# Kernel tuning notes

Hardware: AMD Instinct MI355X
Metric: run time of the kernel (lower is better)

The kernel has to match this reference:

```python
import jax, jax.numpy as jnp
import numpy as np

# Brevitas-style per-tensor affine (symmetric) quantization:
#   scale = max|x| / qmax  (stats-derived, treated as constant)
#   q     = clamp(round(x/scale), qmin, qmax) * scale

def _quant_pt(x, bits):
    qmax = 2.0 ** (bits - 1) - 1.0
    qmin = -(2.0 ** (bits - 1))
    scale = jax.lax.stop_gradient(jnp.max(jnp.abs(x))) / qmax
    scale = jnp.maximum(scale, jnp.asarray(1e-8, x.dtype))
    q = jnp.clip(jnp.round(x / scale), qmin, qmax)
    return q * scale, scale


def setup_inputs() -> dict:
    key = jax.random.key(0)
    k1, k2, k3 = jax.random.split(key, 3)
    in_features, out_features, tokens = 4096, 4096, 8192
    inp = jax.random.normal(k1, (tokens, in_features), dtype=jnp.float32)
    # Kaiming-ish init for linear weight [out, in]
    W = jax.random.normal(k2, (out_features, in_features), dtype=jnp.float32) / np.sqrt(in_features)
    b = jax.random.normal(k3, (out_features,), dtype=jnp.float32) * 0.01
    return {"inp": inp, "W": W, "b": b}


def reference(inp, W, b):
    # input quant: Int8 act per-tensor (QuantIdentity default)
    x_dq, s_in = _quant_pt(inp, 8)
    # weight quant: 4-bit per-tensor
    w_dq, s_w = _quant_pt(W, 4)
    # bias quant: Int32 with scale = s_in * s_w
    s_b = s_in * s_w
    b_dq = jnp.round(b / s_b) * s_b  # int32 range never clips realistic biases
    # matmul in dequantized domain (numerically equal to int GEMM * s_in*s_w)
    y = jnp.einsum('ti,oi->to', x_dq, w_dq) + b_dq
    # output quant: Int8 act per-tensor
    y_dq, _ = _quant_pt(y, 8)
    return y_dq
```

## Files before the change

kernel.cpp:

```cpp
#include <hip/hip_runtime.h>


typedef int v4i __attribute__((ext_vector_type(4)));

#define AS1(p) ((const __attribute__((address_space(1))) void*)(p))
#define AS3(p) ((__attribute__((address_space(3))) void*)(p))

#define GM 8192
#define GN 4096
#define GK 4096
#define NBN 16
#define NWG 512

__global__ __launch_bounds__(256) void maxabs_kernel(const float* __restrict__ x, int n4,
                                                     unsigned* __restrict__ slot) {
  __shared__ float red[4];
  int tid = blockIdx.x * blockDim.x + threadIdx.x;
  int stride = gridDim.x * blockDim.x;
  float m = 0.0f;
  const float4* x4 = (const float4*)x;
  for (int i = tid; i < n4; i += stride) {
    float4 v = x4[i];
    m = fmaxf(m, fmaxf(fmaxf(fabsf(v.x), fabsf(v.y)), fmaxf(fabsf(v.z), fabsf(v.w))));
  }
  for (int off = 32; off; off >>= 1) m = fmaxf(m, __shfl_xor(m, off));
  if ((threadIdx.x & 63) == 0) red[threadIdx.x >> 6] = m;
  __syncthreads();
  if (threadIdx.x == 0) {
    float b = fmaxf(fmaxf(red[0], red[1]), fmaxf(red[2], red[3]));
    atomicMax(slot, __float_as_uint(b));
  }
}

__global__ __launch_bounds__(256) void quant_kernel(const float* __restrict__ x,
                                                    signed char* __restrict__ q, int n4,
                                                    const unsigned* __restrict__ slot,
                                                    float qmaxv, float qlo, float qhi) {
  float s = fmaxf(__uint_as_float(*slot) / qmaxv, 1e-8f);
  float inv = 1.0f / s;
  int tid = blockIdx.x * blockDim.x + threadIdx.x;
  int stride = gridDim.x * blockDim.x;
  const float4* x4 = (const float4*)x;
  int* q4 = (int*)q;
  for (int i = tid; i < n4; i += stride) {
    float4 v = x4[i];
    int a0 = (int)fminf(fmaxf(rintf(v.x * inv), qlo), qhi);
    int a1 = (int)fminf(fmaxf(rintf(v.y * inv), qlo), qhi);
    int a2 = (int)fminf(fmaxf(rintf(v.z * inv), qlo), qhi);
    int a3 = (int)fminf(fmaxf(rintf(v.w * inv), qlo), qhi);
    q4[i] = (a0 & 255) | ((a1 & 255) << 8) | ((a2 & 255) << 16) | ((a3 & 255) << 24);
  }
}

__global__ __launch_bounds__(512, 2) void gemm_i8_kernel(const signed char* __restrict__ Xq,
                                                         const signed char* __restrict__ Wq,
                                                         const float* __restrict__ bias,
                                                         const unsigned* __restrict__ slots,
                                                         float* __restrict__ Y,
                                                         unsigned* __restrict__ maxY) {
  __shared__ signed char smem[131072];
  const int tid = threadIdx.x;
  const int wid = tid >> 6, lane = tid & 63;
  const int wr = wid >> 2, wc = wid & 3;
  const int lr = lane & 15, lg = lane >> 4;

  const int bid = (int)blockIdx.x;
  const int swz = (bid & 7) * (NWG / 8) + (bid >> 3);
  const int brow = (swz / NBN) * 256;
  const int bcol = (swz % NBN) * 256;

  const int srr = tid >> 3;
  const int sgl = (tid & 7) ^ (srr & 7);

#define ASLOT(db, h) (smem + ((db) * 2 + (h)) * 16384)
#define BSLOT(db, h) (smem + 65536 + ((db) * 2 + (h)) * 16384)
#define STAGE(gptr, grow0, kofs, slot)                                                        \
  {                                                                                           \
    const signed char* _s0 = (gptr) + (size_t)((grow0) + srr) * GK + (kofs) + sgl * 16;       \
    __builtin_amdgcn_global_load_lds(AS1(_s0), AS3((slot) + wid * 1024), 16, 0, 0);           \
    __builtin_amdgcn_global_load_lds(AS1(_s0 + (size_t)64 * GK),                              \
                                     AS3((slot) + 8192 + wid * 1024), 16, 0, 0);              \
  }

  STAGE(Xq, brow, 0, ASLOT(0, 0));
  STAGE(Wq, bcol, 0, BSLOT(0, 0));
  STAGE(Xq, brow + 128, 0, ASLOT(0, 1));
  STAGE(Wq, bcol + 128, 0, BSLOT(0, 1));
  STAGE(Xq, brow, 128, ASLOT(1, 0));
  STAGE(Wq, bcol, 128, BSLOT(1, 0));

  v4i acc[8][4] = {};

#pragma unroll 2
  for (int t = 0; t < 32; ++t) {
    const int db = t & 1;
    if (t == 31)
      asm volatile("s_waitcnt vmcnt(0)" ::: "memory");
    else
      asm volatile("s_waitcnt vmcnt(4)" ::: "memory");
    __builtin_amdgcn_s_barrier();
#pragma unroll
    for (int q = 0; q < 4; ++q) {
      const int mh = q >> 1, nh = q & 1;
      const signed char* Abuf = ASLOT(db, mh);
      const signed char* Bbuf = BSLOT(db, nh);
      v4i af[4][2], bf[2][2];
#pragma unroll
      for (int mm = 0; mm < 4; ++mm) {
        int hr = wr * 64 + mm * 16 + lr;
        int sw = hr & 7;
#pragma unroll
        for (int kk = 0; kk < 2; ++kk)
          af[mm][kk] = *(const v4i*)(Abuf + hr * 128 + (((kk * 4 + lg) ^ sw) << 4));
      }
#pragma unroll
      for (int nn = 0; nn < 2; ++nn) {
        int hr = wc * 32 + nn * 16 + lr;
        int sw = hr & 7;
#pragma unroll
        for (int kk = 0; kk < 2; ++kk)
          bf[nn][kk] = *(const v4i*)(Bbuf + hr * 128 + (((kk * 4 + lg) ^ sw) << 4));
      }
      if (q == 0 && t + 1 < 32) STAGE(Xq, brow + 128, (t + 1) * 128, ASLOT((t + 1) & 1, 1));
      if (q == 1 && t + 1 < 32) STAGE(Wq, bcol + 128, (t + 1) * 128, BSLOT((t + 1) & 1, 1));
      if (q == 2 && t + 2 < 32) STAGE(Xq, brow, (t + 2) * 128, ASLOT(db, 0));
      if (q == 3 && t + 2 < 32) STAGE(Wq, bcol, (t + 2) * 128, BSLOT(db, 0));
      __builtin_amdgcn_s_barrier();
      asm volatile("s_waitcnt lgkmcnt(0)");
      __builtin_amdgcn_s_setprio(1);
#pragma unroll
      for (int mm = 0; mm < 4; ++mm)
#pragma unroll
        for (int nn = 0; nn < 2; ++nn)
#pragma unroll
          for (int kk = 0; kk < 2; ++kk)
            acc[mh * 4 + mm][nh * 2 + nn] = __builtin_amdgcn_mfma_i32_16x16x64_i8(
                af[mm][kk], bf[nn][kk], acc[mh * 4 + mm][nh * 2 + nn], 0, 0, 0);
      __builtin_amdgcn_s_setprio(0);
      __builtin_amdgcn_s_barrier();
    }
  }

  float s_in = fmaxf(__uint_as_float(slots[0]) / 127.0f, 1e-8f);
  float s_w = fmaxf(__uint_as_float(slots[1]) / 7.0f, 1e-8f);
  float s_b = s_in * s_w;
  float lmax = 0.0f;
#pragma unroll
  for (int n = 0; n < 4; ++n) {
    int o = bcol + (n >> 1) * 128 + wc * 32 + (n & 1) * 16 + lr;
    float bdq = rintf(bias[o] / s_b) * s_b;
#pragma unroll
    for (int m = 0; m < 8; ++m) {
      int t0 = brow + (m >> 2) * 128 + wr * 64 + (m & 3) * 16 + (lg << 2);
#pragma unroll
      for (int r2 = 0; r2 < 4; ++r2) {
        float yv = (float)acc[m][n][r2] * s_b + bdq;
        Y[(size_t)(t0 + r2) * GN + o] = yv;
        lmax = fmaxf(lmax, fabsf(yv));
      }
    }
  }
  for (int off = 32; off; off >>= 1) lmax = fmaxf(lmax, __shfl_xor(lmax, off));
  float* fred = (float*)smem;
  if (lane == 0) fred[wid] = lmax;
  __syncthreads();
  if (tid == 0) {
    float m = fred[0];
#pragma unroll
    for (int i = 1; i < 8; ++i) m = fmaxf(m, fred[i]);
    atomicMax(maxY, __float_as_uint(m));
  }
#undef STAGE
#undef ASLOT
#undef BSLOT
}

__global__ __launch_bounds__(256) void quant_out_kernel(float* __restrict__ y, int n4,
                                                        const unsigned* __restrict__ slot) {
  float s = fmaxf(__uint_as_float(*slot) / 127.0f, 1e-8f);
  float inv = 1.0f / s;
  int tid = blockIdx.x * blockDim.x + threadIdx.x;
  int stride = gridDim.x * blockDim.x;
  float4* y4 = (float4*)y;
  for (int i = tid; i < n4; i += stride) {
    float4 v = y4[i];
    v.x = fminf(fmaxf(rintf(v.x * inv), -128.0f), 127.0f) * s;
    v.y = fminf(fmaxf(rintf(v.y * inv), -128.0f), 127.0f) * s;
    v.z = fminf(fmaxf(rintf(v.z * inv), -128.0f), 127.0f) * s;
    v.w = fminf(fmaxf(rintf(v.w * inv), -128.0f), 127.0f) * s;
    y4[i] = v;
  }
}

extern "C" void kernel_launch(void* const* d_in, const int* in_sizes, int n_in,
                              void* d_out, int out_size, void* d_ws, size_t ws_size,
                              hipStream_t stream) {
  const float* inp = (const float*)d_in[0];
  const float* W = (const float*)d_in[1];
  const float* b = (const float*)d_in[2];
  float* out = (float*)d_out;

  unsigned* slots = (unsigned*)d_ws;
  signed char* Xq = (signed char*)d_ws + 256;
  signed char* Wq = Xq + (size_t)GM * GK;

  const int nX = GM * GK;
  const int nW = GN * GK;

  hipMemsetAsync(d_ws, 0, 16, stream);

  maxabs_kernel<<<1024, 256, 0, stream>>>(inp, nX / 4, slots + 0);
  maxabs_kernel<<<512, 256, 0, stream>>>(W, nW / 4, slots + 1);

  quant_kernel<<<1024, 256, 0, stream>>>(inp, Xq, nX / 4, slots + 0, 127.0f, -128.0f, 127.0f);
  quant_kernel<<<512, 256, 0, stream>>>(W, Wq, nW / 4, slots + 1, 7.0f, -8.0f, 7.0f);

  gemm_i8_kernel<<<NWG, 512, 0, stream>>>(Xq, Wq, b, slots, out, slots + 2);

  quant_out_kernel<<<1024, 256, 0, stream>>>(out, (GM * GN) / 4, slots + 2);
}
```

Before: 286.0 us.

## Restructure int8 GEMM main loop into k-split phases with reused B fragments

Reorders the GEMM inner loop into four phases split by K-half, not by M/N quadrant. B fragments for all four N sub-tiles are loaded once per K-half and reused across both M halves, which cuts LDS reads. Prefetch changes from a two-deep lookahead to a one-ahead double buffer, with stage issues spread across the phases and a vmcnt(2) wait. Shared-memory address offsets are precomputed. The shallower prefetch may expose more global-load latency.

```diff
diff --git a/kernel.cpp b/kernel.cpp
--- a/kernel.cpp
+++ b/kernel.cpp
@@ -72,6 +72,20 @@
   const int srr = tid >> 3;
   const int sgl = (tid & 7) ^ (srr & 7);
 
+  int aoff[4], asw[4], boff[4], bsw[4];
+#pragma unroll
+  for (int mm = 0; mm < 4; ++mm) {
+    int hr = wr * 64 + mm * 16 + lr;
+    aoff[mm] = hr * 128;
+    asw[mm] = hr & 7;
+  }
+#pragma unroll
+  for (int nn = 0; nn < 4; ++nn) {
+    int hr = wc * 32 + (nn & 1) * 16 + lr;
+    boff[nn] = hr * 128;
+    bsw[nn] = hr & 7;
+  }
+
 #define ASLOT(db, h) (smem + ((db) * 2 + (h)) * 16384)
 #define BSLOT(db, h) (smem + 65536 + ((db) * 2 + (h)) * 16384)
 #define STAGE(gptr, grow0, kofs, slot)                                                        \
@@ -81,64 +95,68 @@
     __builtin_amdgcn_global_load_lds(AS1(_s0 + (size_t)64 * GK),                              \
                                      AS3((slot) + 8192 + wid * 1024), 16, 0, 0);              \
   }
-
+#define LDA(mm, db, h, kk) \
+  *(const v4i*)(ASLOT(db, h) + aoff[mm] + ((((kk)*4 + lg) ^ asw[mm]) << 4))
+#define LDB(nn, db, kk) \
+  *(const v4i*)(BSLOT(db, (nn) >> 1) + boff[nn] + ((((kk)*4 + lg) ^ bsw[nn]) << 4))
+#define MFMA16(arow)                                                                          \
+  __builtin_amdgcn_s_setprio(1);                                                              \
+  _Pragma("unroll") for (int mm = 0; mm < 4; ++mm)                                            \
+      _Pragma("unroll") for (int nn = 0; nn < 4; ++nn)                                        \
+          acc[(arow) + mm][nn] =                                                              \
+      __builtin_amdgcn_mfma_i32_16x16x64_i8(af[mm], bf[nn], acc[(arow) + mm][nn], 0, 0, 0);   \
+  __builtin_amdgcn_s_setprio(0);
+
+  STAGE(Wq, bcol, 0, BSLOT(0, 0));
+  STAGE(Wq, bcol + 128, 0, BSLOT(0, 1));
   STAGE(Xq, brow, 0, ASLOT(0, 0));
-  STAGE(Wq, bcol, 0, BSLOT(0, 0));
   STAGE(Xq, brow + 128, 0, ASLOT(0, 1));
-  STAGE(Wq, bcol + 128, 0, BSLOT(0, 1));
-  STAGE(Xq, brow, 128, ASLOT(1, 0));
-  STAGE(Wq, bcol, 128, BSLOT(1, 0));
 
   v4i acc[8][4] = {};
 
 #pragma unroll 2
   for (int t = 0; t < 32; ++t) {
-    const int db = t & 1;
+    const int db = t & 1, ndb = db ^ 1;
+    const int kof = (t + 1) * 128;
+    v4i af[4], bf[4];
+
+    if (t < 31) STAGE(Wq, bcol, kof, BSLOT(ndb, 0));
     if (t == 31)
       asm volatile("s_waitcnt vmcnt(0)" ::: "memory");
     else
-      asm volatile("s_waitcnt vmcnt(4)" ::: "memory");
-    __builtin_amdgcn_s_barrier();
-#pragma unroll
-    for (int q = 0; q < 4; ++q) {
-      const int mh = q >> 1, nh = q & 1;
-      const signed char* Abuf = ASLOT(db, mh);
-      const signed char* Bbuf = BSLOT(db, nh);
-      v4i af[4][2], bf[2][2];
-#pragma unroll
-      for (int mm = 0; mm < 4; ++mm) {
-        int hr = wr * 64 + mm * 16 + lr;
-        int sw = hr & 7;
-#pragma unroll
-        for (int kk = 0; kk < 2; ++kk)
-          af[mm][kk] = *(const v4i*)(Abuf + hr * 128 + (((kk * 4 + lg) ^ sw) << 4));
-      }
-#pragma unroll
-      for (int nn = 0; nn < 2; ++nn) {
-        int hr = wc * 32 + nn * 16 + lr;
-        int sw = hr & 7;
-#pragma unroll
-        for (int kk = 0; kk < 2; ++kk)
-          bf[nn][kk] = *(const v4i*)(Bbuf + hr * 128 + (((kk * 4 + lg) ^ sw) << 4));
-      }
-      if (q == 0 && t + 1 < 32) STAGE(Xq, brow + 128, (t + 1) * 128, ASLOT((t + 1) & 1, 1));
-      if (q == 1 && t + 1 < 32) STAGE(Wq, bcol + 128, (t + 1) * 128, BSLOT((t + 1) & 1, 1));
-      if (q == 2 && t + 2 < 32) STAGE(Xq, brow, (t + 2) * 128, ASLOT(db, 0));
-      if (q == 3 && t + 2 < 32) STAGE(Wq, bcol, (t + 2) * 128, BSLOT(db, 0));
-      __builtin_amdgcn_s_barrier();
-      asm volatile("s_waitcnt lgkmcnt(0)");
-      __builtin_amdgcn_s_setprio(1);
-#pragma unroll
-      for (int mm = 0; mm < 4; ++mm)
-#pragma unroll
-        for (int nn = 0; nn < 2; ++nn)
-#pragma unroll
-          for (int kk = 0; kk < 2; ++kk)
-            acc[mh * 4 + mm][nh * 2 + nn] = __builtin_amdgcn_mfma_i32_16x16x64_i8(
-                af[mm][kk], bf[nn][kk], acc[mh * 4 + mm][nh * 2 + nn], 0, 0, 0);
-      __builtin_amdgcn_s_setprio(0);
-      __builtin_amdgcn_s_barrier();
-    }
+      asm volatile("s_waitcnt vmcnt(2)" ::: "memory");
+    __builtin_amdgcn_s_barrier();
+
+#pragma unroll
+    for (int mm = 0; mm < 4; ++mm) af[mm] = LDA(mm, db, 0, 0);
+#pragma unroll
+    for (int nn = 0; nn < 4; ++nn) bf[nn] = LDB(nn, db, 0);
+    if (t < 31) STAGE(Wq, bcol + 128, kof, BSLOT(ndb, 1));
+    asm volatile("s_waitcnt lgkmcnt(0)");
+    MFMA16(0)
+    __builtin_amdgcn_s_barrier();
+
+#pragma unroll
+    for (int mm = 0; mm < 4; ++mm) af[mm] = LDA(mm, db, 1, 0);
+    if (t < 31) STAGE(Xq, brow, kof, ASLOT(ndb, 0));
+    asm volatile("s_waitcnt lgkmcnt(0)");
+    MFMA16(4)
+    __builtin_amdgcn_s_barrier();
+
+#pragma unroll
+    for (int mm = 0; mm < 4; ++mm) af[mm] = LDA(mm, db, 0, 1);
+#pragma unroll
+    for (int nn = 0; nn < 4; ++nn) bf[nn] = LDB(nn, db, 1);
+    if (t < 31) STAGE(Xq, brow + 128, kof, ASLOT(ndb, 1));
+    asm volatile("s_waitcnt lgkmcnt(0)");
+    MFMA16(0)
+    __builtin_amdgcn_s_barrier();
+
+#pragma unroll
+    for (int mm = 0; mm < 4; ++mm) af[mm] = LDA(mm, db, 1, 1);
+    asm volatile("s_waitcnt lgkmcnt(0)");
+    MFMA16(4)
+    __builtin_amdgcn_s_barrier();
   }
 
   float s_in = fmaxf(__uint_as_float(slots[0]) / 127.0f, 1e-8f);
@@ -173,6 +191,9 @@
 #undef STAGE
 #undef ASLOT
 #undef BSLOT
+#undef LDA
+#undef LDB
+#undef MFMA16
 }
 
 __global__ __launch_bounds__(256) void quant_out_kernel(float* __restrict__ y, int n4,
```

Measured after the change: 265.9 us. -7.0%, faster.
